# Performance work log

Measured on AMD Instinct MI355X. Metric: run time of the kernel, lower is better.

## Reference

```python
import jax, jax.numpy as jnp
import numpy as np

N = 100000      # nodes
E = 800000      # edges (before self loops)
D_IN = 128
D_H = 128
HEADS = 8
HD = D_H // HEADS   # per-head dim for hidden layers
D_OUT = 64
SLOPE = 0.2         # PyG GATConv default negative_slope
EPS_BN = 1e-5
EPS_LN = 1e-5


def setup_inputs() -> dict:
    key = jax.random.key(0)
    ks = jax.random.split(key, 20)
    def p(k, shape, scale=0.1):
        return jax.random.normal(k, shape, dtype=jnp.float32) * scale
    inp = {
        "x": jax.random.normal(ks[0], (N, D_IN), dtype=jnp.float32),
        "edge_index": jax.random.randint(ks[1], (2, E), 0, N, dtype=jnp.int32),
        # GATConv 0: 128 -> 8 heads x 16, concat -> 128
        "W0": p(ks[2], (D_IN, D_H)), "as0": p(ks[3], (HEADS, HD)), "ad0": p(ks[4], (HEADS, HD)),
        "b0": jnp.zeros((D_H,), jnp.float32),
        "g0": jnp.ones((D_H,), jnp.float32), "bt0": jnp.zeros((D_H,), jnp.float32),
        # GATConv 1: 128 -> 8 heads x 16, concat -> 128
        "W1": p(ks[5], (D_H, D_H)), "as1": p(ks[6], (HEADS, HD)), "ad1": p(ks[7], (HEADS, HD)),
        "b1": jnp.zeros((D_H,), jnp.float32),
        "g1": jnp.ones((D_H,), jnp.float32), "bt1": jnp.zeros((D_H,), jnp.float32),
        # GATConv 2 (final): 128 -> 1 head x 64, no concat
        "W2": p(ks[8], (D_H, D_OUT)), "as2": p(ks[9], (1, D_OUT)), "ad2": p(ks[10], (1, D_OUT)),
        "b2": jnp.zeros((D_OUT,), jnp.float32),
        # output LayerNorm
        "ln_g": jnp.ones((D_OUT,), jnp.float32), "ln_b": jnp.zeros((D_OUT,), jnp.float32),
    }
    return inp


def gat_conv(x, src, dst, W, a_s, a_d, heads):
    """PyG-style GATConv (eval mode, self loops already in src/dst).
    Returns [N, heads, head_dim]."""
    n = x.shape[0]
    h = (x @ W).reshape(n, heads, -1)              # [N, H, D]
    al_s = jnp.sum(h * a_s, axis=-1)               # [N, H]
    al_d = jnp.sum(h * a_d, axis=-1)               # [N, H]
    e = jax.nn.leaky_relu(al_s[src] + al_d[dst], SLOPE)  # [Etot, H]
    # softmax over incoming edges of each destination node
    m = jax.ops.segment_max(e, dst, num_segments=n)
    e = jnp.exp(e - m[dst])
    s = jax.ops.segment_sum(e, dst, num_segments=n)
    alpha = e / (s[dst] + 1e-16)                   # [Etot, H]
    msg = h[src] * alpha[:, :, None]               # [Etot, H, D]
    return jax.ops.segment_sum(msg, dst, num_segments=n)


def batch_norm(x, g, b):
    mu = jnp.mean(x, axis=0)
    var = jnp.var(x, axis=0)
    return (x - mu) * jax.lax.rsqrt(var + EPS_BN) * g + b


def reference(x, edge_index, W0, as0, ad0, b0, g0, bt0,
              W1, as1, ad1, b1, g1, bt1,
              W2, as2, ad2, b2, ln_g, ln_b):
    n = x.shape[0]
    loops = jnp.arange(n, dtype=edge_index.dtype)
    src = jnp.concatenate([edge_index[0], loops])
    dst = jnp.concatenate([edge_index[1], loops])

    # layer 0
    out = gat_conv(x, src, dst, W0, as0, ad0, HEADS).reshape(n, D_H) + b0
    out = jax.nn.relu(batch_norm(out, g0, bt0))
    x = out + x                                    # residual (128 == 128)

    # layer 1
    out = gat_conv(x, src, dst, W1, as1, ad1, HEADS).reshape(n, D_H) + b1
    out = jax.nn.relu(batch_norm(out, g1, bt1))
    x = out + x

    # final layer: 1 head, concat=False
    out = gat_conv(x, src, dst, W2, as2, ad2, 1).reshape(n, D_OUT) + b2

    # output LayerNorm
    mu = jnp.mean(out, axis=-1, keepdims=True)
    var = jnp.var(out, axis=-1, keepdims=True)
    return (out - mu) * jax.lax.rsqrt(var + EPS_LN) * ln_g + ln_b
```

## Files before the change

kernel.cpp:

```cpp
#include <hip/hip_runtime.h>
#include <hip/hip_bf16.h>

#define LRELU(e) ((e) > 0.f ? (e) : 0.2f * (e))

typedef __attribute__((ext_vector_type(8))) short bf16x8;
typedef __attribute__((ext_vector_type(4))) float floatx4;

__device__ inline short f2bf(float f) {
    union { float f; unsigned u; } v; v.f = f;
    unsigned r = v.u + 0x7fffu + ((v.u >> 16) & 1u);
    return (short)(r >> 16);
}
__device__ inline float bflo(int p) {
    union { unsigned u; float f; } v; v.u = (unsigned)p << 16; return v.f;
}
__device__ inline float bfhi(int p) {
    union { unsigned u; float f; } v; v.u = (unsigned)p & 0xffff0000u; return v.f;
}
__device__ inline float bf2f(unsigned short s) {
    union { unsigned u; float f; } v; v.u = (unsigned)s << 16; return v.f;
}


__global__ void k_count_wprep(const int* __restrict__ dstE, int E, int N,
                              int* __restrict__ deg,
                              const float* __restrict__ W0, const float* __restrict__ W1,
                              const float* __restrict__ W2,
                              const float* __restrict__ as0, const float* __restrict__ ad0,
                              const float* __restrict__ as1, const float* __restrict__ ad1,
                              const float* __restrict__ as2, const float* __restrict__ ad2,
                              short* __restrict__ Wt0, short* __restrict__ Wt1,
                              short* __restrict__ Wt2) {
    int i = blockIdx.x * blockDim.x + threadIdx.x;
    if (i < E) atomicAdd(&deg[dstE[i]], 1);
    else if (i < E + N) atomicAdd(&deg[i - E], 1);

    if (i < 128 * 128) {
        int n = i >> 7, k = i & 127;
        Wt0[n * 128 + k] = f2bf(W0[k * 128 + n]);
        Wt1[n * 128 + k] = f2bf(W1[k * 128 + n]);
    } else if (i < 128 * 128 + 64 * 128) {
        int j = i - 128 * 128;
        int n = j >> 7, k = j & 127;
        Wt2[n * 128 + k] = f2bf(W2[k * 64 + n]);
    } else if (i < 128 * 128 + 64 * 128 + 128 * 8) {
        int j = i - (128 * 128 + 64 * 128);
        int k = j >> 3, h = j & 7;
        float s0 = 0.f, d0 = 0.f, s1 = 0.f, d1 = 0.f;
        #pragma unroll
        for (int d = 0; d < 16; d++) {
            float w0 = W0[k * 128 + h * 16 + d];
            float w1 = W1[k * 128 + h * 16 + d];
            s0 += w0 * as0[h * 16 + d];
            d0 += w0 * ad0[h * 16 + d];
            s1 += w1 * as1[h * 16 + d];
            d1 += w1 * ad1[h * 16 + d];
        }
        Wt0[(128 + h) * 128 + k] = f2bf(s0);
        Wt0[(136 + h) * 128 + k] = f2bf(d0);
        Wt1[(128 + h) * 128 + k] = f2bf(s1);
        Wt1[(136 + h) * 128 + k] = f2bf(d1);
    } else if (i < 128 * 128 + 64 * 128 + 128 * 8 + 128) {
        int k = i - (128 * 128 + 64 * 128 + 128 * 8);
        float s = 0.f, d = 0.f;
        #pragma unroll
        for (int dd = 0; dd < 64; dd++) {
            float w = W2[k * 64 + dd];
            s += w * as2[dd];
            d += w * ad2[dd];
        }
        Wt2[64 * 128 + k] = f2bf(s);
        Wt2[65 * 128 + k] = f2bf(d);
        #pragma unroll
        for (int r = 66; r < 80; r++) Wt2[r * 128 + k] = 0;
    }
}

constexpr int SC = 2048;

__global__ __launch_bounds__(256) void k_scan1(const int* __restrict__ deg, int N,
                                               int* __restrict__ partial) {
    int base = blockIdx.x * SC;
    int t = threadIdx.x;
    int s = 0;
    #pragma unroll
    for (int p = 0; p < SC / 256; p++) {
        int i = base + t + p * 256;
        if (i < N) s += deg[i];
    }
    #pragma unroll
    for (int off = 32; off; off >>= 1) s += __shfl_xor(s, off, 64);
    __shared__ int ws[4];
    int lane = t & 63, wid = t >> 6;
    if (lane == 0) ws[wid] = s;
    __syncthreads();
    if (t == 0) partial[blockIdx.x] = ws[0] + ws[1] + ws[2] + ws[3];
}

__global__ __launch_bounds__(256) void k_scan2(int* __restrict__ partial, int nb) {
    int t = threadIdx.x;
    int v = (t < nb) ? partial[t] : 0;
    int lane = t & 63, wid = t >> 6;
    int x = v;
    #pragma unroll
    for (int off = 1; off < 64; off <<= 1) {
        int y = __shfl_up(x, off, 64);
        if (lane >= off) x += y;
    }
    __shared__ int wsum[4];
    if (lane == 63) wsum[wid] = x;
    __syncthreads();
    int add = 0;
    for (int i = 0; i < wid; i++) add += wsum[i];
    if (t < nb) partial[t] = x + add - v;
}


__global__ __launch_bounds__(256) void k_scan3(const int* __restrict__ deg, int N, int Etot,
                                               const int* __restrict__ partial,
                                               int* __restrict__ rowptr,
                                               int* __restrict__ bcursor) {
    int base = blockIdx.x * SC;
    int t = threadIdx.x;
    int i0 = base + t * 8;
    int v[8];
    int s = 0;
    #pragma unroll
    for (int p = 0; p < 8; p++) {
        int i = i0 + p;
        v[p] = (i < N) ? deg[i] : 0;
        s += v[p];
    }
    int lane = t & 63, wid = t >> 6;
    int x = s;
    #pragma unroll
    for (int off = 1; off < 64; off <<= 1) {
        int y = __shfl_up(x, off, 64);
        if (lane >= off) x += y;
    }
    __shared__ int wsum[4];
    if (lane == 63) wsum[wid] = x;
    __syncthreads();
    int add = 0;
    for (int i = 0; i < wid; i++) add += wsum[i];
    int excl = x - s + add + partial[blockIdx.x];
    #pragma unroll
    for (int p = 0; p < 8; p++) {
        int i = i0 + p;
        if (i < N) {
            rowptr[i] = excl;
            if ((i & 127) == 0) bcursor[i >> 7] = excl - i;
        }
        excl += v[p];
    }
    if (blockIdx.x == 0 && t == 0) rowptr[N] = Etot;
}


constexpr int EPT = 16;

__global__ __launch_bounds__(256) void k_bin(const int* __restrict__ srcE,
                                             const int* __restrict__ dstE, int E, int nb,
                                             int* __restrict__ bcursor,
                                             int2* __restrict__ ebin) {
    __shared__ int cnt[1024];
    __shared__ int base[1024];
    for (int b = threadIdx.x; b < nb; b += 256) cnt[b] = 0;
    __syncthreads();
    int i0 = blockIdx.x * (256 * EPT) + threadIdx.x;
    int rb[EPT];
    #pragma unroll
    for (int k = 0; k < EPT; k++) {
        int i = i0 + k * 256;
        if (i < E) {
            int b = dstE[i] >> 7;
            rb[k] = (atomicAdd(&cnt[b], 1) << 10) | b;
        } else {
            rb[k] = -1;
        }
    }
    __syncthreads();
    for (int b = threadIdx.x; b < nb; b += 256) {
        int c = cnt[b];
        base[b] = c ? atomicAdd(&bcursor[b], c) : 0;
    }
    __syncthreads();
    #pragma unroll
    for (int k = 0; k < EPT; k++) {
        int i = i0 + k * 256;
        if (i < E) {
            int v = rb[k];
            int b = v & 1023;
            int r = v >> 10;
            ebin[base[b] + r] = make_int2(srcE[i], dstE[i]);
        }
    }
}


__global__ __launch_bounds__(256) void k_cfill(const int* __restrict__ rowptr,
                                               const int2* __restrict__ ebin,
                                               int* __restrict__ col, int N) {
    int n0 = blockIdx.x << 7;
    int nn = N - n0; if (nn > 128) nn = 128;
    __shared__ int cur[128];
    __shared__ int eb[2];
    int t = threadIdx.x;
    if (t <= nn) {
        int rp = rowptr[n0 + t];
        if (t < nn) {
            col[rp] = n0 + t;
            cur[t] = rp + 1;
        }
        if (t == 0) eb[0] = rp - n0;
        if (t == nn) eb[1] = rp - (n0 + nn);
    }
    __syncthreads();
    int ebase = eb[0];
    int ecnt = eb[1] - ebase;
    for (int i = t; i < ecnt; i += 256) {
        int2 e = ebin[ebase + i];
        int p = atomicAdd(&cur[e.y - n0], 1);
        col[p] = e.x;
    }
}


template <int DOUT, bool HASBN, bool RESBF16, bool WRITEX>
__global__ __launch_bounds__(256) void k_gemm(const void* __restrict__ Xv,
                                              const short* __restrict__ Wt,
                                              short* __restrict__ Hout,
                                              const float2* __restrict__ ss,
                                              const void* __restrict__ Xresv,
                                              short* __restrict__ Xout,
                                              float* __restrict__ als,
                                              float* __restrict__ ald, int Nrows) {
    constexpr int KP = 136;
    constexpr int CT = DOUT / 16;
    constexpr int CTT = CT + 1;
    __shared__ __align__(16) short Xs[128 * KP];
    __shared__ __align__(16) short Ws[(DOUT + 16) * KP];

    const int tid = threadIdx.x;
    const int row0 = blockIdx.x * 128;

    {
        int c4 = tid & 31;
        int r0 = tid >> 5;
        float2 ssv[4];
        if (HASBN) {
            #pragma unroll
            for (int j = 0; j < 4; j++) ssv[j] = ss[c4 * 4 + j];
        }
        #pragma unroll
        for (int p = 0; p < 16; p++) {
            int r = r0 + p * 8;
            int grow = row0 + r;
            float vp[4] = {0.f, 0.f, 0.f, 0.f};
            if (grow < Nrows) {
                if (HASBN) {
                    short4 xb = *(const short4*)&((const short*)Xv)[(size_t)grow * 128 + c4 * 4];
                    vp[0] = bf2f((unsigned short)xb.x);
                    vp[1] = bf2f((unsigned short)xb.y);
                    vp[2] = bf2f((unsigned short)xb.z);
                    vp[3] = bf2f((unsigned short)xb.w);
                    float xr[4];
                    if (RESBF16) {
                        short4 rb = *(const short4*)&((const short*)Xresv)[(size_t)grow * 128 + c4 * 4];
                        xr[0] = bf2f((unsigned short)rb.x);
                        xr[1] = bf2f((unsigned short)rb.y);
                        xr[2] = bf2f((unsigned short)rb.z);
                        xr[3] = bf2f((unsigned short)rb.w);
                    } else {
                        float4 rf = *(const float4*)&((const float*)Xresv)[(size_t)grow * 128 + c4 * 4];
                        xr[0] = rf.x; xr[1] = rf.y; xr[2] = rf.z; xr[3] = rf.w;
                    }
                    #pragma unroll
                    for (int j = 0; j < 4; j++)
                        vp[j] = fmaxf(vp[j] * ssv[j].x + ssv[j].y, 0.f) + xr[j];
                } else {
                    float4 v = *(const float4*)&((const float*)Xv)[(size_t)grow * 128 + c4 * 4];
                    vp[0] = v.x; vp[1] = v.y; vp[2] = v.z; vp[3] = v.w;
                }
            }
            short4 b;
            b.x = f2bf(vp[0]); b.y = f2bf(vp[1]); b.z = f2bf(vp[2]); b.w = f2bf(vp[3]);
            if (WRITEX && grow < Nrows)
                *(short4*)&Xout[(size_t)grow * 128 + c4 * 4] = b;
            *(short4*)&Xs[r * KP + c4 * 4] = b;
        }
    }
    {
        constexpr int UNITS = (DOUT + 16) * 16;
        #pragma unroll
        for (int p = 0; p < UNITS / 256; p++) {
            int u = tid + p * 256;
            int n = u >> 4;
            int kc = (u & 15) * 8;
            bf16x8 v = *(const bf16x8*)&Wt[n * 128 + kc];
            *(bf16x8*)&Ws[n * KP + kc] = v;
        }
    }
    __syncthreads();

    const int lane = tid & 63;
    const int wv = tid >> 6;
    const int m0 = wv * 32;
    const int ln = lane & 15;
    const int quad = lane >> 4;

    floatx4 acc[2][CTT];
    #pragma unroll
    for (int mt = 0; mt < 2; mt++)
        #pragma unroll
        for (int ct = 0; ct < CTT; ct++) acc[mt][ct] = (floatx4){0.f, 0.f, 0.f, 0.f};

    #pragma unroll
    for (int ks = 0; ks < 4; ks++) {
        int ko = ks * 32 + quad * 8;
        bf16x8 a0 = *(const bf16x8*)&Xs[(m0 + ln) * KP + ko];
        bf16x8 a1 = *(const bf16x8*)&Xs[(m0 + 16 + ln) * KP + ko];
        #pragma unroll
        for (int ct = 0; ct < CTT; ct++) {
            bf16x8 b = *(const bf16x8*)&Ws[(ct * 16 + ln) * KP + ko];
            acc[0][ct] = __builtin_amdgcn_mfma_f32_16x16x32_bf16(a0, b, acc[0][ct], 0, 0, 0);
            acc[1][ct] = __builtin_amdgcn_mfma_f32_16x16x32_bf16(a1, b, acc[1][ct], 0, 0, 0);
        }
    }

    #pragma unroll
    for (int mt = 0; mt < 2; mt++) {
        #pragma unroll
        for (int r = 0; r < 4; r++) {
            int grow = row0 + m0 + mt * 16 + quad * 4 + r;
            if (grow < Nrows) {
                #pragma unroll
                for (int ct = 0; ct < CT; ct++)
                    Hout[(size_t)grow * DOUT + ct * 16 + ln] = f2bf(acc[mt][ct][r]);
                float aug = acc[mt][CT][r];
                if (DOUT == 128) {
                    if (ln < 8) als[grow * 8 + ln] = aug;
                    else        ald[grow * 8 + (ln - 8)] = aug;
                } else {
                    if (ln == 0) als[grow] = aug;
                    else if (ln == 1) ald[grow] = aug;
                }
            }
        }
    }
}


__global__ __launch_bounds__(256) void k_agg(const int* __restrict__ rowptr,
                                             const int* __restrict__ col,
                                             const short* __restrict__ Hb,
                                             const float* __restrict__ als,
                                             const float* __restrict__ ald,
                                             const float* __restrict__ bias,
                                             short* __restrict__ out,
                                             float* __restrict__ part, int N) {
    __shared__ float red[8][128];
    int wv = threadIdx.x >> 6;
    int lane = threadIdx.x & 63;
    int nodeA = blockIdx.x * 8 + wv * 2;
    int nodeB = nodeA + 1;
    int h = lane >> 3;
    const int* Hi = (const int*)Hb;
    bool vA = nodeA < N, vB = nodeB < N;
    int jA = 0, endA = 0, jB = 0, endB = 0;
    float aldA = 0.f, aldB = 0.f;
    if (vA) { jA = rowptr[nodeA]; endA = rowptr[nodeA + 1]; aldA = ald[nodeA * 8 + h]; }
    if (vB) { jB = rowptr[nodeB]; endB = rowptr[nodeB + 1]; aldB = ald[nodeB * 8 + h]; }
    float sA = 0.f, a0A = 0.f, a1A = 0.f;
    float sB = 0.f, a0B = 0.f, a1B = 0.f;

    while (jA + 4 <= endA && jB + 4 <= endB) {
        int c[8];
        #pragma unroll
        for (int k = 0; k < 4; k++) { c[k] = col[jA + k]; c[4 + k] = col[jB + k]; }
        float aw[8];
        int p[8];
        #pragma unroll
        for (int k = 0; k < 4; k++) {
            aw[k] = als[c[k] * 8 + h];
            aw[4 + k] = als[c[4 + k] * 8 + h];
            p[k] = Hi[(c[k] << 6) + lane];
            p[4 + k] = Hi[(c[4 + k] << 6) + lane];
        }
        #pragma unroll
        for (int k = 0; k < 4; k++) {
            float e = aw[k] + aldA; e = LRELU(e); float w = __expf(e);
            sA += w;  a0A += w * bflo(p[k]);  a1A += w * bfhi(p[k]);
            float e2 = aw[4 + k] + aldB; e2 = LRELU(e2); float w2 = __expf(e2);
            sB += w2; a0B += w2 * bflo(p[4 + k]); a1B += w2 * bfhi(p[4 + k]);
        }
        jA += 4; jB += 4;
    }
    for (; jA + 4 <= endA; jA += 4) {
        int c[4]; float aw[4]; int p[4];
        #pragma unroll
        for (int k = 0; k < 4; k++) c[k] = col[jA + k];
        #pragma unroll
        for (int k = 0; k < 4; k++) { aw[k] = als[c[k] * 8 + h]; p[k] = Hi[(c[k] << 6) + lane]; }
        #pragma unroll
        for (int k = 0; k < 4; k++) {
            float e = aw[k] + aldA; e = LRELU(e); float w = __expf(e);
            sA += w; a0A += w * bflo(p[k]); a1A += w * bfhi(p[k]);
        }
    }
    for (; jA < endA; jA++) {
        int cc = col[jA];
        float e = als[cc * 8 + h] + aldA; e = LRELU(e); float w = __expf(e);
        int pp = Hi[(cc << 6) + lane];
        sA += w; a0A += w * bflo(pp); a1A += w * bfhi(pp);
    }
    for (; jB + 4 <= endB; jB += 4) {
        int c[4]; float aw[4]; int p[4];
        #pragma unroll
        for (int k = 0; k < 4; k++) c[k] = col[jB + k];
        #pragma unroll
        for (int k = 0; k < 4; k++) { aw[k] = als[c[k] * 8 + h]; p[k] = Hi[(c[k] << 6) + lane]; }
        #pragma unroll
        for (int k = 0; k < 4; k++) {
            float e = aw[k] + aldB; e = LRELU(e); float w = __expf(e);
            sB += w; a0B += w * bflo(p[k]); a1B += w * bfhi(p[k]);
        }
    }
    for (; jB < endB; jB++) {
        int cc = col[jB];
        float e = als[cc * 8 + h] + aldB; e = LRELU(e); float w = __expf(e);
        int pp = Hi[(cc << 6) + lane];
        sB += w; a0B += w * bflo(pp); a1B += w * bfhi(pp);
    }

    float bx = bias[2 * lane], by = bias[2 * lane + 1];
    float2 oA = make_float2(0.f, 0.f), oB = make_float2(0.f, 0.f);
    if (vA) {
        float inv = 1.f / (sA + 1e-16f);
        oA.x = a0A * inv + bx;
        oA.y = a1A * inv + by;
        int pack = (unsigned short)f2bf(oA.x) | ((unsigned)(unsigned short)f2bf(oA.y) << 16);
        ((int*)out)[(size_t)nodeA * 64 + lane] = pack;
    }
    if (vB) {
        float inv = 1.f / (sB + 1e-16f);
        oB.x = a0B * inv + bx;
        oB.y = a1B * inv + by;
        int pack = (unsigned short)f2bf(oB.x) | ((unsigned)(unsigned short)f2bf(oB.y) << 16);
        ((int*)out)[(size_t)nodeB * 64 + lane] = pack;
    }
    red[wv * 2][2 * lane] = oA.x;
    red[wv * 2][2 * lane + 1] = oA.y;
    red[wv * 2 + 1][2 * lane] = oB.x;
    red[wv * 2 + 1][2 * lane + 1] = oB.y;
    __syncthreads();
    if (threadIdx.x < 128) {
        int c = threadIdx.x;
        float s = 0.f, q = 0.f;
        #pragma unroll
        for (int r = 0; r < 8; r++) {
            float v = red[r][c];
            s += v;
            q += v * v;
        }
        float* slot = part + (blockIdx.x & 63) * 256;
        atomicAdd(&slot[c], s);
        atomicAdd(&slot[128 + c], q);
    }
}


__global__ __launch_bounds__(128) void k_bnreduce(float* __restrict__ part,
                                                  const float* __restrict__ g,
                                                  const float* __restrict__ bt,
                                                  float invN, float2* __restrict__ ss) {
    int c = threadIdx.x;
    float s = 0.f, q = 0.f;
    #pragma unroll
    for (int k = 0; k < 64; k++) {
        s += part[k * 256 + c];
        q += part[k * 256 + 128 + c];
    }
    #pragma unroll
    for (int k = 0; k < 64; k++) {
        part[k * 256 + c] = 0.f;
        part[k * 256 + 128 + c] = 0.f;
    }
    float mu = s * invN;
    float var = q * invN - mu * mu;
    float scale = rsqrtf(var + 1e-5f) * g[c];
    ss[c] = make_float2(scale, bt[c] - mu * scale);
}


__global__ __launch_bounds__(256) void k_agg2ln(const int* __restrict__ rowptr,
                                                const int* __restrict__ col,
                                                const short* __restrict__ Hb2,
                                                const float* __restrict__ als,
                                                const float* __restrict__ ald,
                                                const float* __restrict__ b2,
                                                const float* __restrict__ lng,
                                                const float* __restrict__ lnb,
                                                float* __restrict__ out, int N) {
    int wv = threadIdx.x >> 6;
    int lane = threadIdx.x & 63;
    int nodeA = blockIdx.x * 8 + wv * 2;
    int nodeB = nodeA + 1;
    const unsigned short* H = (const unsigned short*)Hb2;
    bool vA = nodeA < N, vB = nodeB < N;
    int jA = 0, endA = 0, jB = 0, endB = 0;
    float aldA = 0.f, aldB = 0.f;
    if (vA) { jA = rowptr[nodeA]; endA = rowptr[nodeA + 1]; aldA = ald[nodeA]; }
    if (vB) { jB = rowptr[nodeB]; endB = rowptr[nodeB + 1]; aldB = ald[nodeB]; }
    float sA = 0.f, aA = 0.f, sB = 0.f, aB = 0.f;

    while (jA + 4 <= endA && jB + 4 <= endB) {
        int c[8];
        #pragma unroll
        for (int k = 0; k < 4; k++) { c[k] = col[jA + k]; c[4 + k] = col[jB + k]; }
        float aw[8];
        unsigned short p[8];
        #pragma unroll
        for (int k = 0; k < 4; k++) {
            aw[k] = als[c[k]];
            aw[4 + k] = als[c[4 + k]];
            p[k] = H[(c[k] << 6) + lane];
            p[4 + k] = H[(c[4 + k] << 6) + lane];
        }
        #pragma unroll
        for (int k = 0; k < 4; k++) {
            float e = aw[k] + aldA; e = LRELU(e); float w = __expf(e);
            sA += w; aA += w * bf2f(p[k]);
            float e2 = aw[4 + k] + aldB; e2 = LRELU(e2); float w2 = __expf(e2);
            sB += w2; aB += w2 * bf2f(p[4 + k]);
        }
        jA += 4; jB += 4;
    }
    for (; jA + 4 <= endA; jA += 4) {
        int c[4]; float aw[4]; unsigned short p[4];
        #pragma unroll
        for (int k = 0; k < 4; k++) c[k] = col[jA + k];
        #pragma unroll
        for (int k = 0; k < 4; k++) { aw[k] = als[c[k]]; p[k] = H[(c[k] << 6) + lane]; }
        #pragma unroll
        for (int k = 0; k < 4; k++) {
            float e = aw[k] + aldA; e = LRELU(e); float w = __expf(e);
            sA += w; aA += w * bf2f(p[k]);
        }
    }
    for (; jA < endA; jA++) {
        int cc = col[jA];
        float e = als[cc] + aldA; e = LRELU(e); float w = __expf(e);
        sA += w; aA += w * bf2f(H[(cc << 6) + lane]);
    }
    for (; jB + 4 <= endB; jB += 4) {
        int c[4]; float aw[4]; unsigned short p[4];
        #pragma unroll
        for (int k = 0; k < 4; k++) c[k] = col[jB + k];
        #pragma unroll
        for (int k = 0; k < 4; k++) { aw[k] = als[c[k]]; p[k] = H[(c[k] << 6) + lane]; }
        #pragma unroll
        for (int k = 0; k < 4; k++) {
            float e = aw[k] + aldB; e = LRELU(e); float w = __expf(e);
            sB += w; aB += w * bf2f(p[k]);
        }
    }
    for (; jB < endB; jB++) {
        int cc = col[jB];
        float e = als[cc] + aldB; e = LRELU(e); float w = __expf(e);
        sB += w; aB += w * bf2f(H[(cc << 6) + lane]);
    }

    if (vA) {
        float v = aA / (sA + 1e-16f) + b2[lane];
        float su = v, sq = v * v;
        #pragma unroll
        for (int off = 32; off; off >>= 1) {
            su += __shfl_xor(su, off, 64);
            sq += __shfl_xor(sq, off, 64);
        }
        float mu = su * (1.f / 64.f);
        float var = sq * (1.f / 64.f) - mu * mu;
        float r = rsqrtf(var + 1e-5f);
        out[(size_t)nodeA * 64 + lane] = (v - mu) * r * lng[lane] + lnb[lane];
    }
    if (vB) {
        float v = aB / (sB + 1e-16f) + b2[lane];
        float su = v, sq = v * v;
        #pragma unroll
        for (int off = 32; off; off >>= 1) {
            su += __shfl_xor(su, off, 64);
            sq += __shfl_xor(sq, off, 64);
        }
        float mu = su * (1.f / 64.f);
        float var = sq * (1.f / 64.f) - mu * mu;
        float r = rsqrtf(var + 1e-5f);
        out[(size_t)nodeB * 64 + lane] = (v - mu) * r * lng[lane] + lnb[lane];
    }
}


extern "C" void kernel_launch(void* const* d_in, const int* in_sizes, int n_in,
                              void* d_out, int out_size, void* d_ws, size_t ws_size,
                              hipStream_t stream) {
    const float* x   = (const float*)d_in[0];
    const int*   ei  = (const int*)d_in[1];
    const float* W0  = (const float*)d_in[2];
    const float* as0 = (const float*)d_in[3];
    const float* ad0 = (const float*)d_in[4];
    const float* b0  = (const float*)d_in[5];
    const float* g0  = (const float*)d_in[6];
    const float* bt0 = (const float*)d_in[7];
    const float* W1  = (const float*)d_in[8];
    const float* as1 = (const float*)d_in[9];
    const float* ad1 = (const float*)d_in[10];
    const float* b1  = (const float*)d_in[11];
    const float* g1  = (const float*)d_in[12];
    const float* bt1 = (const float*)d_in[13];
    const float* W2  = (const float*)d_in[14];
    const float* as2 = (const float*)d_in[15];
    const float* ad2 = (const float*)d_in[16];
    const float* b2  = (const float*)d_in[17];
    const float* lng = (const float*)d_in[18];
    const float* lnb = (const float*)d_in[19];

    const int N = in_sizes[0] / 128;
    const int E = in_sizes[1] / 2;
    const int Etot = E + N;
    const int nb = (N + 127) >> 7;

    char* p = (char*)d_ws;
    auto carve = [&](size_t bytes) {
        void* q = (void*)p;
        p += (bytes + 255) & ~(size_t)255;
        return q;
    };
    short* Hb     = (short*)carve((size_t)N * 128 * 2);
    short* aggb   = (short*)carve((size_t)N * 128 * 2);
    short* x1b    = (short*)carve((size_t)N * 128 * 2);
    float* als    = (float*)carve((size_t)N * 8 * 4);
    float* ald    = (float*)carve((size_t)N * 8 * 4);
    int*   rowptr = (int*)carve((size_t)(N + 1) * 4);
    const size_t degpad = ((size_t)N * 4 + 255) & ~(size_t)255;
    int*   deg    = (int*)carve(degpad);
    float* part   = (float*)carve(64 * 256 * 4);
    int*   col    = (int*)carve((size_t)Etot * 4);
    int2*  ebin   = (int2*)carve((size_t)E * 8);
    int*   bcursor= (int*)carve(1024 * 4);
    float2* ss    = (float2*)carve(128 * 8);
    short* Wt0    = (short*)carve(144 * 128 * 2);
    short* Wt1    = (short*)carve(144 * 128 * 2);
    short* Wt2    = (short*)carve(80 * 128 * 2);
    int*   partial= (int*)carve(256 * 4);

    const float invN = 1.f / (float)N;
    const int eb = (E + N + 255) / 256;
    const int nsb = (N + SC - 1) / SC;

    hipMemsetAsync(deg, 0, degpad + 64 * 256 * 4, stream);
    k_count_wprep<<<eb, 256, 0, stream>>>(ei + E, E, N, deg, W0, W1, W2,
                                          as0, ad0, as1, ad1, as2, ad2, Wt0, Wt1, Wt2);
    k_scan1<<<nsb, 256, 0, stream>>>(deg, N, partial);
    k_scan2<<<1, 256, 0, stream>>>(partial, nsb);
    k_scan3<<<nsb, 256, 0, stream>>>(deg, N, Etot, partial, rowptr, bcursor);
    const int bb = (E + 256 * EPT - 1) / (256 * EPT);
    k_bin<<<bb, 256, 0, stream>>>(ei, ei + E, E, nb, bcursor, ebin);
    k_cfill<<<nb, 256, 0, stream>>>(rowptr, ebin, col, N);

    const int gb = (N + 127) / 128;
    const int ab = (N + 7) / 8;

    k_gemm<128, false, false, false><<<gb, 256, 0, stream>>>(x, Wt0, Hb, nullptr, nullptr,
                                                             nullptr, als, ald, N);
    k_agg<<<ab, 256, 0, stream>>>(rowptr, col, Hb, als, ald, b0, aggb, part, N);
    k_bnreduce<<<1, 128, 0, stream>>>(part, g0, bt0, invN, ss);

    k_gemm<128, true, false, true><<<gb, 256, 0, stream>>>(aggb, Wt1, Hb, ss, x, x1b,
                                                           als, ald, N);
    k_agg<<<ab, 256, 0, stream>>>(rowptr, col, Hb, als, ald, b1, aggb, part, N);
    k_bnreduce<<<1, 128, 0, stream>>>(part, g1, bt1, invN, ss);

    k_gemm<64, true, true, false><<<gb, 256, 0, stream>>>(aggb, Wt2, Hb, ss, x1b, nullptr,
                                                          als, ald, N);
    k_agg2ln<<<ab, 256, 0, stream>>>(rowptr, col, Hb, als, ald, b2, lng, lnb,
                                     (float*)d_out, N);
}
```

Measured before the change: 428.9 us.

## Split each wavefront into two half-waves, one node each, with wider per-lane loads

The aggregation kernels now give each 32-lane half of a wavefront its own destination node. Each lane loads 8 bytes (4 bf16) in the hidden layers, or 4 bytes (2 bf16) in the final layer, and the edge loop runs with a predicated step of two edges until no lane has work left. This replaces the earlier scheme where a full wave handled two nodes in sequence, with a paired 4-edge loop plus scalar tails, and is meant to cut tail and serialization overhead while widening memory accesses. The cost is wasted work when the two nodes in a wave have unequal degrees, plus clamped duplicate loads on predicated-off steps.

```diff
diff --git a/kernel.cpp b/kernel.cpp
--- a/kernel.cpp
+++ b/kernel.cpp
@@ -360,111 +360,78 @@
                                              short* __restrict__ out,
                                              float* __restrict__ part, int N) {
     __shared__ float red[8][128];
-    int wv = threadIdx.x >> 6;
-    int lane = threadIdx.x & 63;
-    int nodeA = blockIdx.x * 8 + wv * 2;
-    int nodeB = nodeA + 1;
-    int h = lane >> 3;
-    const int* Hi = (const int*)Hb;
-    bool vA = nodeA < N, vB = nodeB < N;
-    int jA = 0, endA = 0, jB = 0, endB = 0;
-    float aldA = 0.f, aldB = 0.f;
-    if (vA) { jA = rowptr[nodeA]; endA = rowptr[nodeA + 1]; aldA = ald[nodeA * 8 + h]; }
-    if (vB) { jB = rowptr[nodeB]; endB = rowptr[nodeB + 1]; aldB = ald[nodeB * 8 + h]; }
-    float sA = 0.f, a0A = 0.f, a1A = 0.f;
-    float sB = 0.f, a0B = 0.f, a1B = 0.f;
-
-    while (jA + 4 <= endA && jB + 4 <= endB) {
-        int c[8];
-        #pragma unroll
-        for (int k = 0; k < 4; k++) { c[k] = col[jA + k]; c[4 + k] = col[jB + k]; }
-        float aw[8];
-        int p[8];
-        #pragma unroll
-        for (int k = 0; k < 4; k++) {
-            aw[k] = als[c[k] * 8 + h];
-            aw[4 + k] = als[c[4 + k] * 8 + h];
-            p[k] = Hi[(c[k] << 6) + lane];
-            p[4 + k] = Hi[(c[4 + k] << 6) + lane];
-        }
-        #pragma unroll
-        for (int k = 0; k < 4; k++) {
-            float e = aw[k] + aldA; e = LRELU(e); float w = __expf(e);
-            sA += w;  a0A += w * bflo(p[k]);  a1A += w * bfhi(p[k]);
-            float e2 = aw[4 + k] + aldB; e2 = LRELU(e2); float w2 = __expf(e2);
-            sB += w2; a0B += w2 * bflo(p[4 + k]); a1B += w2 * bfhi(p[4 + k]);
-        }
-        jA += 4; jB += 4;
-    }
-    for (; jA + 4 <= endA; jA += 4) {
-        int c[4]; float aw[4]; int p[4];
-        #pragma unroll
-        for (int k = 0; k < 4; k++) c[k] = col[jA + k];
-        #pragma unroll
-        for (int k = 0; k < 4; k++) { aw[k] = als[c[k] * 8 + h]; p[k] = Hi[(c[k] << 6) + lane]; }
-        #pragma unroll
-        for (int k = 0; k < 4; k++) {
-            float e = aw[k] + aldA; e = LRELU(e); float w = __expf(e);
-            sA += w; a0A += w * bflo(p[k]); a1A += w * bfhi(p[k]);
-        }
-    }
-    for (; jA < endA; jA++) {
-        int cc = col[jA];
-        float e = als[cc * 8 + h] + aldA; e = LRELU(e); float w = __expf(e);
-        int pp = Hi[(cc << 6) + lane];
-        sA += w; a0A += w * bflo(pp); a1A += w * bfhi(pp);
-    }
-    for (; jB + 4 <= endB; jB += 4) {
-        int c[4]; float aw[4]; int p[4];
-        #pragma unroll
-        for (int k = 0; k < 4; k++) c[k] = col[jB + k];
-        #pragma unroll
-        for (int k = 0; k < 4; k++) { aw[k] = als[c[k] * 8 + h]; p[k] = Hi[(c[k] << 6) + lane]; }
-        #pragma unroll
-        for (int k = 0; k < 4; k++) {
-            float e = aw[k] + aldB; e = LRELU(e); float w = __expf(e);
-            sB += w; a0B += w * bflo(p[k]); a1B += w * bfhi(p[k]);
-        }
-    }
-    for (; jB < endB; jB++) {
-        int cc = col[jB];
-        float e = als[cc * 8 + h] + aldB; e = LRELU(e); float w = __expf(e);
-        int pp = Hi[(cc << 6) + lane];
-        sB += w; a0B += w * bflo(pp); a1B += w * bfhi(pp);
-    }
-
-    float bx = bias[2 * lane], by = bias[2 * lane + 1];
-    float2 oA = make_float2(0.f, 0.f), oB = make_float2(0.f, 0.f);
-    if (vA) {
-        float inv = 1.f / (sA + 1e-16f);
-        oA.x = a0A * inv + bx;
-        oA.y = a1A * inv + by;
-        int pack = (unsigned short)f2bf(oA.x) | ((unsigned)(unsigned short)f2bf(oA.y) << 16);
-        ((int*)out)[(size_t)nodeA * 64 + lane] = pack;
-    }
-    if (vB) {
-        float inv = 1.f / (sB + 1e-16f);
-        oB.x = a0B * inv + bx;
-        oB.y = a1B * inv + by;
-        int pack = (unsigned short)f2bf(oB.x) | ((unsigned)(unsigned short)f2bf(oB.y) << 16);
-        ((int*)out)[(size_t)nodeB * 64 + lane] = pack;
-    }
-    red[wv * 2][2 * lane] = oA.x;
-    red[wv * 2][2 * lane + 1] = oA.y;
-    red[wv * 2 + 1][2 * lane] = oB.x;
-    red[wv * 2 + 1][2 * lane + 1] = oB.y;
+    const int wv = threadIdx.x >> 6;
+    const int lane = threadIdx.x & 63;
+    const int g = lane >> 5;
+    const int f = lane & 31;
+    const int h = f >> 2;
+    const int node = blockIdx.x * 8 + wv * 2 + g;
+    const int2* H2 = (const int2*)Hb;
+
+    int j, end;
+    float aldv;
+    if (node < N) {
+        j = rowptr[node];
+        end = rowptr[node + 1];
+        aldv = ald[node * 8 + h];
+    } else {
+        j = 1; end = 1; aldv = 0.f;
+    }
+    float s = 0.f, a0 = 0.f, a1 = 0.f, a2 = 0.f, a3 = 0.f;
+
+    while (__any(j < end)) {
+        bool v0 = j < end, v1 = j + 1 < end;
+        int ci0 = v0 ? j : end - 1;
+        int ci1 = v1 ? j + 1 : end - 1;
+        int c0 = col[ci0];
+        int c1 = col[ci1];
+        float aw0 = als[c0 * 8 + h];
+        float aw1 = als[c1 * 8 + h];
+        int2 p0 = H2[(c0 << 5) + f];
+        int2 p1 = H2[(c1 << 5) + f];
+        float e0 = aw0 + aldv; e0 = LRELU(e0);
+        float e1 = aw1 + aldv; e1 = LRELU(e1);
+        float w0 = v0 ? __expf(e0) : 0.f;
+        float w1 = v1 ? __expf(e1) : 0.f;
+        s += w0;
+        a0 += w0 * bflo(p0.x); a1 += w0 * bfhi(p0.x);
+        a2 += w0 * bflo(p0.y); a3 += w0 * bfhi(p0.y);
+        s += w1;
+        a0 += w1 * bflo(p1.x); a1 += w1 * bfhi(p1.x);
+        a2 += w1 * bflo(p1.y); a3 += w1 * bfhi(p1.y);
+        j += 2;
+    }
+
+    float o0 = 0.f, o1 = 0.f, o2 = 0.f, o3 = 0.f;
+    if (node < N) {
+        float4 bv = ((const float4*)bias)[f];
+        float inv = 1.f / (s + 1e-16f);
+        o0 = a0 * inv + bv.x;
+        o1 = a1 * inv + bv.y;
+        o2 = a2 * inv + bv.z;
+        o3 = a3 * inv + bv.w;
+        int2 pk;
+        pk.x = (int)((unsigned short)f2bf(o0) | ((unsigned)(unsigned short)f2bf(o1) << 16));
+        pk.y = (int)((unsigned short)f2bf(o2) | ((unsigned)(unsigned short)f2bf(o3) << 16));
+        ((int2*)out)[(size_t)node * 32 + f] = pk;
+    }
+    const int rrow = wv * 2 + g;
+    red[rrow][4 * f + 0] = o0;
+    red[rrow][4 * f + 1] = o1;
+    red[rrow][4 * f + 2] = o2;
+    red[rrow][4 * f + 3] = o3;
     __syncthreads();
     if (threadIdx.x < 128) {
         int c = threadIdx.x;
-        float s = 0.f, q = 0.f;
+        float s2 = 0.f, q = 0.f;
         #pragma unroll
         for (int r = 0; r < 8; r++) {
             float v = red[r][c];
-            s += v;
+            s2 += v;
             q += v * v;
         }
         float* slot = part + (blockIdx.x & 63) * 256;
-        atomicAdd(&slot[c], s);
+        atomicAdd(&slot[c], s2);
         atomicAdd(&slot[128 + c], q);
     }
 }
@@ -502,101 +469,64 @@
                                                 const float* __restrict__ lng,
                                                 const float* __restrict__ lnb,
                                                 float* __restrict__ out, int N) {
-    int wv = threadIdx.x >> 6;
-    int lane = threadIdx.x & 63;
-    int nodeA = blockIdx.x * 8 + wv * 2;
-    int nodeB = nodeA + 1;
-    const unsigned short* H = (const unsigned short*)Hb2;
-    bool vA = nodeA < N, vB = nodeB < N;
-    int jA = 0, endA = 0, jB = 0, endB = 0;
-    float aldA = 0.f, aldB = 0.f;
-    if (vA) { jA = rowptr[nodeA]; endA = rowptr[nodeA + 1]; aldA = ald[nodeA]; }
-    if (vB) { jB = rowptr[nodeB]; endB = rowptr[nodeB + 1]; aldB = ald[nodeB]; }
-    float sA = 0.f, aA = 0.f, sB = 0.f, aB = 0.f;
-
-    while (jA + 4 <= endA && jB + 4 <= endB) {
-        int c[8];
-        #pragma unroll
-        for (int k = 0; k < 4; k++) { c[k] = col[jA + k]; c[4 + k] = col[jB + k]; }
-        float aw[8];
-        unsigned short p[8];
-        #pragma unroll
-        for (int k = 0; k < 4; k++) {
-            aw[k] = als[c[k]];
-            aw[4 + k] = als[c[4 + k]];
-            p[k] = H[(c[k] << 6) + lane];
-            p[4 + k] = H[(c[4 + k] << 6) + lane];
-        }
-        #pragma unroll
-        for (int k = 0; k < 4; k++) {
-            float e = aw[k] + aldA; e = LRELU(e); float w = __expf(e);
-            sA += w; aA += w * bf2f(p[k]);
-            float e2 = aw[4 + k] + aldB; e2 = LRELU(e2); float w2 = __expf(e2);
-            sB += w2; aB += w2 * bf2f(p[4 + k]);
-        }
-        jA += 4; jB += 4;
-    }
-    for (; jA + 4 <= endA; jA += 4) {
-        int c[4]; float aw[4]; unsigned short p[4];
-        #pragma unroll
-        for (int k = 0; k < 4; k++) c[k] = col[jA + k];
-        #pragma unroll
-        for (int k = 0; k < 4; k++) { aw[k] = als[c[k]]; p[k] = H[(c[k] << 6) + lane]; }
-        #pragma unroll
-        for (int k = 0; k < 4; k++) {
-            float e = aw[k] + aldA; e = LRELU(e); float w = __expf(e);
-            sA += w; aA += w * bf2f(p[k]);
-        }
-    }
-    for (; jA < endA; jA++) {
-        int cc = col[jA];
-        float e = als[cc] + aldA; e = LRELU(e); float w = __expf(e);
-        sA += w; aA += w * bf2f(H[(cc << 6) + lane]);
-    }
-    for (; jB + 4 <= endB; jB += 4) {
-        int c[4]; float aw[4]; unsigned short p[4];
-        #pragma unroll
-        for (int k = 0; k < 4; k++) c[k] = col[jB + k];
-        #pragma unroll
-        for (int k = 0; k < 4; k++) { aw[k] = als[c[k]]; p[k] = H[(c[k] << 6) + lane]; }
-        #pragma unroll
-        for (int k = 0; k < 4; k++) {
-            float e = aw[k] + aldB; e = LRELU(e); float w = __expf(e);
-            sB += w; aB += w * bf2f(p[k]);
-        }
-    }
-    for (; jB < endB; jB++) {
-        int cc = col[jB];
-        float e = als[cc] + aldB; e = LRELU(e); float w = __expf(e);
-        sB += w; aB += w * bf2f(H[(cc << 6) + lane]);
-    }
-
-    if (vA) {
-        float v = aA / (sA + 1e-16f) + b2[lane];
-        float su = v, sq = v * v;
-        #pragma unroll
-        for (int off = 32; off; off >>= 1) {
-            su += __shfl_xor(su, off, 64);
-            sq += __shfl_xor(sq, off, 64);
-        }
-        float mu = su * (1.f / 64.f);
-        float var = sq * (1.f / 64.f) - mu * mu;
-        float r = rsqrtf(var + 1e-5f);
-        out[(size_t)nodeA * 64 + lane] = (v - mu) * r * lng[lane] + lnb[lane];
-    }
-    if (vB) {
-        float v = aB / (sB + 1e-16f) + b2[lane];
-        float su = v, sq = v * v;
-        #pragma unroll
-        for (int off = 32; off; off >>= 1) {
-            su += __shfl_xor(su, off, 64);
-            sq += __shfl_xor(sq, off, 64);
-        }
-        float mu = su * (1.f / 64.f);
-        float var = sq * (1.f / 64.f) - mu * mu;
-        float r = rsqrtf(var + 1e-5f);
-        out[(size_t)nodeB * 64 + lane] = (v - mu) * r * lng[lane] + lnb[lane];
-    }
+    const int wv = threadIdx.x >> 6;
+    const int lane = threadIdx.x & 63;
+    const int g = lane >> 5;
+    const int f = lane & 31;
+    const int node = blockIdx.x * 8 + wv * 2 + g;
+    const int* H1 = (const int*)Hb2;
+    const bool vn = node < N;
+
+    int j, end;
+    float aldv;
+    if (vn) {
+        j = rowptr[node];
+        end = rowptr[node + 1];
+        aldv = ald[node];
+    } else {
+        j = 1; end = 1; aldv = 0.f;
+    }
+    float s = 0.f, a0 = 0.f, a1 = 0.f;
+
+    while (__any(j < end)) {
+        bool v0 = j < end, v1 = j + 1 < end;
+        int ci0 = v0 ? j : end - 1;
+        int ci1 = v1 ? j + 1 : end - 1;
+        int c0 = col[ci0];
+        int c1 = col[ci1];
+        float aw0 = als[c0];
+        float aw1 = als[c1];
+        int p0 = H1[(c0 << 5) + f];
+        int p1 = H1[(c1 << 5) + f];
+        float e0 = aw0 + aldv; e0 = LRELU(e0);
+        float e1 = aw1 + aldv; e1 = LRELU(e1);
+        float w0 = v0 ? __expf(e0) : 0.f;
+        float w1 = v1 ? __expf(e1) : 0.f;
+        s += w0; a0 += w0 * bflo(p0); a1 += w0 * bfhi(p0);
+        s += w1; a0 += w1 * bflo(p1); a1 += w1 * bfhi(p1);
+        j += 2;
+    }
+
+    if (!vn) return;
+    float inv = 1.f / (s + 1e-16f);
+    float2 bv = ((const float2*)b2)[f];
+    float v0 = a0 * inv + bv.x;
+    float v1 = a1 * inv + bv.y;
+    float su = v0 + v1, sq = v0 * v0 + v1 * v1;
+    #pragma unroll
+    for (int off = 1; off < 32; off <<= 1) {
+        su += __shfl_xor(su, off, 64);
+        sq += __shfl_xor(sq, off, 64);
+    }
+    float mu = su * (1.f / 64.f);
+    float var = sq * (1.f / 64.f) - mu * mu;
+    float r = rsqrtf(var + 1e-5f);
+    float2 lg = ((const float2*)lng)[f];
+    float2 lb = ((const float2*)lnb)[f];
+    float2 ov;
+    ov.x = (v0 - mu) * r * lg.x + lb.x;
+    ov.y = (v1 - mu) * r * lg.y + lb.y;
+    ((float2*)out)[(size_t)node * 32 + f] = ov;
 }
 
 
```

New measurement: 430.0 us. No clear change (+0.3%).
